# Performance work log

Measured on AMD Instinct MI355X. Metric: run time of the kernel, lower is better.

## Reference

```python
import jax, jax.numpy as jnp
import numpy as np

H = 512      # hidden_dim
OPS = 12     # num_ops
E = 112      # total_edges = num_cells * sum(i+2 for i in range(num_nodes)) = 8*14


def setup_inputs() -> dict:
    key = jax.random.key(0)
    ks = jax.random.split(key, 16)
    s = lambda k, shape: jax.random.normal(k, shape, dtype=jnp.float32) * 0.05
    return {
        "temperature": 1,
        "h0": s(ks[0], (2, H)),
        "c0": s(ks[1], (2, H)),
        "Wih0": s(ks[2], (4 * H, H)),
        "Whh0": s(ks[3], (4 * H, H)),
        "bih0": s(ks[4], (4 * H,)),
        "bhh0": s(ks[5], (4 * H,)),
        "Wih1": s(ks[6], (4 * H, H)),
        "Whh1": s(ks[7], (4 * H, H)),
        "bih1": s(ks[8], (4 * H,)),
        "bhh1": s(ks[9], (4 * H,)),
        "emb": s(ks[10], (OPS, H)),
        "cW1": s(ks[11], (E, H, H)),
        "cb1": s(ks[12], (E, H)),
        "cW2": s(ks[13], (E, H, OPS)),
        "cb2": s(ks[14], (E, OPS)),
    }


def _lstm_cell(x, h, c, Wih, Whh, bih, bhh):
    # PyTorch LSTM gate order: i, f, g, o
    gates = x @ Wih.T + bih + h @ Whh.T + bhh  # [4H]
    i, f, g, o = jnp.split(gates, 4)
    c2 = jax.nn.sigmoid(f) * c + jax.nn.sigmoid(i) * jnp.tanh(g)
    h2 = jax.nn.sigmoid(o) * jnp.tanh(c2)
    return h2, c2


def reference(temperature, h0, c0, Wih0, Whh0, bih0, bhh0,
              Wih1, Whh1, bih1, bhh1, emb, cW1, cb1, cW2, cb2):
    temp = jnp.asarray(temperature, jnp.float32)
    # Gumbel-max trick == torch Categorical sampling (fixed on-device noise)
    gumbel = jax.random.gumbel(jax.random.key(42), (E, OPS), dtype=jnp.float32)

    def step(carry, xs):
        h, c, prev_action = carry          # h, c: [2, H]
        idx, W1, b1, W2, b2, gnoise = xs
        x = jnp.where(idx == 0, jnp.zeros((H,), jnp.float32), emb[prev_action])
        h0n, c0n = _lstm_cell(x, h[0], c[0], Wih0, Whh0, bih0, bhh0)
        h1n, c1n = _lstm_cell(h0n, h[1], c[1], Wih1, Whh1, bih1, bhh1)
        hmlp = jax.nn.relu(h1n @ W1 + b1)   # controller hidden
        logits = (hmlp @ W2 + b2) / temp    # [OPS]
        logp = jax.nn.log_softmax(logits)
        action = jnp.argmax(logits + gnoise).astype(jnp.int32)
        lp = logp[action]
        ent = -jnp.sum(jnp.exp(logp) * logp)
        new_carry = (jnp.stack([h0n, h1n]), jnp.stack([c0n, c1n]), action)
        return new_carry, (action, lp, ent)

    init = (h0, c0, jnp.int32(0))
    xs = (jnp.arange(E), cW1, cb1, cW2, cb2, gumbel)
    _, (actions, log_probs, entropies) = jax.lax.scan(step, init, xs)
    return actions, log_probs, entropies
```

## Files before the change

kernel.cpp:

```cpp
#include <hip/hip_runtime.h>
#include <math.h>

#define H    512
#define OPS  12
#define E    112
#define NWG  128
#define NT   256

typedef unsigned long long u64;

#define TW_BASE  16
#define TW_HB0   0
#define TW_HB1   1024
#define TW_HMB   2048
#define TW_TOTAL 3072

__device__ __forceinline__ float sigf(float x) { return 1.f / (1.f + expf(-x)); }

__device__ __forceinline__ void threefry_42(unsigned x0, unsigned x1,
                                            unsigned& o0, unsigned& o1) {
  const unsigned k0 = 0u, k1 = 42u;
  const unsigned k2 = k0 ^ k1 ^ 0x1BD11BDAu;
  x0 += k0; x1 += k1;
#define TF_R(rot) { x0 += x1; x1 = (x1 << rot) | (x1 >> (32 - rot)); x1 ^= x0; }
  TF_R(13) TF_R(15) TF_R(26) TF_R(6)
  x0 += k1; x1 += k2 + 1u;
  TF_R(17) TF_R(29) TF_R(16) TF_R(24)
  x0 += k2; x1 += k0 + 2u;
  TF_R(13) TF_R(15) TF_R(26) TF_R(6)
  x0 += k0; x1 += k1 + 3u;
  TF_R(17) TF_R(29) TF_R(16) TF_R(24)
  x0 += k1; x1 += k2 + 4u;
  TF_R(13) TF_R(15) TF_R(26) TF_R(6)
  x0 += k2; x1 += k0 + 5u;
#undef TF_R
  o0 = x0; o1 = x1;
}

__device__ __forceinline__ float bits_to_gumbel(unsigned bits) {
  unsigned fb = (bits >> 9) | 0x3f800000u;
  float u = __uint_as_float(fb) - 1.0f;
  u = u + 1.17549435e-38f;
  u = fmaxf(1.17549435e-38f, u);
  return -logf(-logf(u));
}

__device__ __forceinline__ float decode_temp(const void* temp_p) {
  float tf = *(const float*)temp_p;
  float a = fabsf(tf);
  if (a > 1e-6f && a < 1e6f) return tf;
  int ti = *(const int*)temp_p;
  if (ti != 0 && ti > -1000000 && ti < 1000000) return (float)ti;
  double td = *(const double*)temp_p;
  double ad = fabs(td);
  if (ad > 1e-6 && ad < 1e6) return (float)td;
  return 1.0f;
}

__device__ __forceinline__ void tag_store(u64* p, unsigned tag, float f) {
  u64 v = ((u64)tag << 32) | (u64)__float_as_uint(f);
  __hip_atomic_store(p, v, __ATOMIC_RELAXED, __HIP_MEMORY_SCOPE_SYSTEM);
}
__device__ __forceinline__ float tag_poll(const u64* p, unsigned tag) {
  u64 v = __hip_atomic_load(p, __ATOMIC_RELAXED, __HIP_MEMORY_SCOPE_SYSTEM);
  while ((unsigned)(v >> 32) != tag) {
    __builtin_amdgcn_s_sleep(1);
    v = __hip_atomic_load(p, __ATOMIC_RELAXED, __HIP_MEMORY_SCOPE_SYSTEM);
  }
  return __uint_as_float((unsigned)v);
}

__global__ void k_init(u64* tw) {
  int t = blockIdx.x * blockDim.x + threadIdx.x;
  if (t < TW_TOTAL) tw[t] = 0ull;
}
__global__ void k_diag(float* out, float v) {
  if (threadIdx.x == 0 && blockIdx.x == 0) out[0] = v;
}

__global__ void __launch_bounds__(NT)
policy_persist(const void* temp_p,
               const float* __restrict__ h0_in, const float* __restrict__ c0_in,
               const float* __restrict__ Wih0,  const float* __restrict__ Whh0,
               const float* __restrict__ bih0,  const float* __restrict__ bhh0,
               const float* __restrict__ Wih1,  const float* __restrict__ Whh1,
               const float* __restrict__ bih1,  const float* __restrict__ bhh1,
               const float* __restrict__ emb,   const float* __restrict__ cW1,
               const float* __restrict__ cb1,   const float* __restrict__ cW2,
               const float* __restrict__ cb2,
               float* __restrict__ out, float* ws) {
  __shared__ __align__(16) float shp0[H], shp1[H], hm[H];
  __shared__ float g0pre[16], g1bpre[16], g1loc[16];
  __shared__ float ewloc[12 * 16], b0loc[16], b1loc[16];
  __shared__ float gum[E * OPS];
  __shared__ float w1s[512 * 5];
  __shared__ float w2s[512 * 13];
  __shared__ float c0loc[4], c1loc[4];
  __shared__ float spart[4][4];
  __shared__ int s_act;

  const int tid = threadIdx.x;
  const int bid = blockIdx.x;
  const int j0  = bid * 4;
  const int cb  = (bid & 7) * 16 + (bid >> 3);
  const float invt = 1.f / decode_temp(temp_p);

  u64* HB0 = (u64*)(ws + TW_BASE) + TW_HB0;
  u64* HB1 = (u64*)(ws + TW_BASE) + TW_HB1;
  u64* HMB = (u64*)(ws + TW_BASE) + TW_HMB;

  for (int p = tid; p < E * OPS; p += NT) {
    unsigned y0, y1;
    threefry_42(0u, (unsigned)p, y0, y1);
    gum[p] = bits_to_gumbel(y0 ^ y1);
  }
  for (int j = tid; j < H; j += NT) {
    shp0[j] = h0_in[j];
    shp1[j] = h0_in[H + j];
  }
  if (tid < 192) {
    int a = tid / 16, ridx = tid % 16;
    int g = ridx >> 2, dj = ridx & 3;
    int row = g * H + j0 + dj;
    const float* er = emb + a * H;
    const float* wr = Wih0 + (size_t)row * H;
    float acc = 0.f;
    for (int k = 0; k < H; k += 4) {
      float4 e4 = *(const float4*)(er + k);
      float4 w4 = *(const float4*)(wr + k);
      acc += e4.x * w4.x + e4.y * w4.y + e4.z * w4.z + e4.w * w4.w;
    }
    ewloc[tid] = acc;
  }
  if (tid < 16) {
    int g = tid >> 2, dj = tid & 3;
    int row = g * H + j0 + dj;
    b0loc[tid] = bih0[row] + bhh0[row];
    b1loc[tid] = bih1[row] + bhh1[row];
  }
  if (tid < 4) {
    c0loc[tid] = c0_in[j0 + tid];
    c1loc[tid] = c0_in[H + j0 + tid];
  }
  __syncthreads();

  {
    int rowidx = tid >> 3, lane = tid & 7;
    int cell = rowidx >> 4, ridx = rowidx & 15;
    int g = ridx >> 2, dj = ridx & 3;
    int row = g * H + j0 + dj;
    const float* wr = (cell ? Whh1 : Whh0) + (size_t)row * H + lane * 64;
    const float* hv = (cell ? shp1 : shp0) + lane * 64;
    float acc = 0.f;
#pragma unroll
    for (int k = 0; k < 64; k += 4) {
      float4 w4 = *(const float4*)(wr + k);
      acc += w4.x * hv[k] + w4.y * hv[k + 1] + w4.z * hv[k + 2] + w4.w * hv[k + 3];
    }
    acc += __shfl_xor(acc, 1);
    acc += __shfl_xor(acc, 2);
    acc += __shfl_xor(acc, 4);
    if (lane == 0) {
      if (cell == 0) g0pre[ridx] = acc + b0loc[ridx];
      else           g1bpre[ridx] = acc;
    }
    const float* wb = cW1 + (size_t)cb * 4;
    float4 r0 = *(const float4*)(wb + (size_t)tid * H);
    float4 r1 = *(const float4*)(wb + (size_t)(tid + 256) * H);
    int k0 = tid * 5, k1 = (tid + 256) * 5;
    w1s[k0] = r0.x; w1s[k0 + 1] = r0.y; w1s[k0 + 2] = r0.z; w1s[k0 + 3] = r0.w;
    w1s[k1] = r1.x; w1s[k1 + 1] = r1.y; w1s[k1 + 2] = r1.z; w1s[k1 + 3] = r1.w;
  }
  __syncthreads();

#pragma unroll 1
  for (int i = 0; i < E; ++i) {
    const int p = i & 1;
    const unsigned tg = (unsigned)(i + 1);

    if (i > 0) {
      const int q = (i - 1) & 1;
      const unsigned tgp = (unsigned)i;
      int t2 = tid * 2;
      hm[t2]     = tag_poll(&HMB[q * 512 + t2],     tgp);
      hm[t2 + 1] = tag_poll(&HMB[q * 512 + t2 + 1], tgp);
      __syncthreads();
      if (tid < 64) {
        float lg[OPS];
#pragma unroll
        for (int o = 0; o < OPS; ++o) lg[o] = 0.f;
#pragma unroll
        for (int jj = 0; jj < 8; ++jj) {
          int j = jj * 64 + tid;
          float hmv = hm[j];
          const float* w2r = &w2s[j * 13];
#pragma unroll
          for (int o = 0; o < OPS; ++o) lg[o] += hmv * w2r[o];
        }
#pragma unroll
        for (int s = 1; s < 64; s <<= 1) {
#pragma unroll
          for (int o = 0; o < OPS; ++o) lg[o] += __shfl_xor(lg[o], s);
        }
#pragma unroll
        for (int o = 0; o < OPS; ++o) lg[o] = (lg[o] + cb2[(i - 1) * OPS + o]) * invt;
        float mx = lg[0];
#pragma unroll
        for (int o = 1; o < OPS; ++o) mx = fmaxf(mx, lg[o]);
        float se = 0.f;
#pragma unroll
        for (int o = 0; o < OPS; ++o) se += expf(lg[o] - mx);
        float logZ = mx + logf(se);
        float best = -1e30f; int act = 0;
#pragma unroll
        for (int o = 0; o < OPS; ++o) {
          float v = lg[o] + gum[(i - 1) * OPS + o];
          if (v > best) { best = v; act = o; }
        }
        if (tid == 0) {
          s_act = act;
          if (bid == 0) {
            float lp = lg[act] - logZ;
            float ent = 0.f;
            for (int o = 0; o < OPS; ++o) {
              float l2 = lg[o] - logZ;
              ent -= expf(l2) * l2;
            }
            out[i - 1]         = (float)act;
            out[E + i - 1]     = lp;
            out[2 * E + i - 1] = ent;
          }
        }
      }
    }

    if (tid < 4) {
      int a = (i > 0) ? s_act : -1;
      float gi = g0pre[tid];
      float gf = g0pre[4 + tid];
      float gg = g0pre[8 + tid];
      float go = g0pre[12 + tid];
      if (a >= 0) {
        gi += ewloc[a * 16 + tid];
        gf += ewloc[a * 16 + 4 + tid];
        gg += ewloc[a * 16 + 8 + tid];
        go += ewloc[a * 16 + 12 + tid];
      }
      float cn = sigf(gf) * c0loc[tid] + sigf(gi) * tanhf(gg);
      c0loc[tid] = cn;
      tag_store(&HB0[p * 512 + j0 + tid], tg, sigf(go) * tanhf(cn));
    }

    {
      int t2 = tid * 2;
      shp0[t2]     = tag_poll(&HB0[p * 512 + t2],     tg);
      shp0[t2 + 1] = tag_poll(&HB0[p * 512 + t2 + 1], tg);
    }
    __syncthreads();

    {
      int ridx = tid >> 4, lane = tid & 15;
      int g = ridx >> 2, dj = ridx & 3;
      int row = g * H + j0 + dj;
      const float* wr = Wih1 + (size_t)row * H + lane * 32;
      const float* hv = shp0 + lane * 32;
      float acc = 0.f;
#pragma unroll
      for (int k = 0; k < 32; k += 4) {
        float4 w4 = *(const float4*)(wr + k);
        acc += w4.x * hv[k] + w4.y * hv[k + 1] + w4.z * hv[k + 2] + w4.w * hv[k + 3];
      }
      acc += __shfl_xor(acc, 1);
      acc += __shfl_xor(acc, 2);
      acc += __shfl_xor(acc, 4);
      acc += __shfl_xor(acc, 8);
      if (lane == 0) g1loc[ridx] = acc + g1bpre[ridx] + b1loc[ridx];
    }
    __syncthreads();

    if (tid < 4) {
      float gi = g1loc[tid];
      float gf = g1loc[4 + tid];
      float gg = g1loc[8 + tid];
      float go = g1loc[12 + tid];
      float cn = sigf(gf) * c1loc[tid] + sigf(gi) * tanhf(gg);
      c1loc[tid] = cn;
      tag_store(&HB1[p * 512 + j0 + tid], tg, sigf(go) * tanhf(cn));
    }

    {
      int t2 = tid * 2;
      shp1[t2]     = tag_poll(&HB1[p * 512 + t2],     tg);
      shp1[t2 + 1] = tag_poll(&HB1[p * 512 + t2 + 1], tg);
    }
    __syncthreads();

    {
      int wv = tid >> 6, ln = tid & 63;
      int jl = ln & 3, ks = ln >> 2;
      int kbase = wv * 128 + ks * 8;
      float acc = 0.f;
#pragma unroll
      for (int t = 0; t < 8; ++t) {
        int k = kbase + t;
        acc += shp1[k] * w1s[k * 5 + jl];
      }
      acc += __shfl_xor(acc, 4);
      acc += __shfl_xor(acc, 8);
      acc += __shfl_xor(acc, 16);
      acc += __shfl_xor(acc, 32);
      if (ln < 4) spart[wv][ln] = acc;
    }
    __syncthreads();
    if (tid < 4) {
      float s = spart[0][tid] + spart[1][tid] + spart[2][tid] + spart[3][tid];
      s += cb1[(size_t)i * H + cb * 4 + tid];
      tag_store(&HMB[p * 512 + cb * 4 + tid], tg, fmaxf(s, 0.f));
    }

    {
      const float* wsrc = cW2 + (size_t)i * H * OPS;
#pragma unroll
      for (int r = 0; r < 6; ++r) {
        int q = tid + 256 * r;
        float4 v = *(const float4*)(wsrc + 4 * q);
        int f = 4 * q;
        w2s[(f / 12) * 13 + (f % 12)]             = v.x;
        w2s[((f + 1) / 12) * 13 + ((f + 1) % 12)] = v.y;
        w2s[((f + 2) / 12) * 13 + ((f + 2) % 12)] = v.z;
        w2s[((f + 3) / 12) * 13 + ((f + 3) % 12)] = v.w;
      }
    }
    if (i + 1 < E) {
      const float* wb = cW1 + (size_t)(i + 1) * H * H + (size_t)cb * 4;
      float4 r0 = *(const float4*)(wb + (size_t)tid * H);
      float4 r1 = *(const float4*)(wb + (size_t)(tid + 256) * H);
      {
        int rowidx = tid >> 3, lane = tid & 7;
        int cell = rowidx >> 4, ridx = rowidx & 15;
        int g = ridx >> 2, dj = ridx & 3;
        int row = g * H + j0 + dj;
        const float* wr = (cell ? Whh1 : Whh0) + (size_t)row * H + lane * 64;
        const float* hv = (cell ? shp1 : shp0) + lane * 64;
        float acc = 0.f;
#pragma unroll
        for (int k = 0; k < 64; k += 4) {
          float4 w4 = *(const float4*)(wr + k);
          acc += w4.x * hv[k] + w4.y * hv[k + 1] + w4.z * hv[k + 2] + w4.w * hv[k + 3];
        }
        acc += __shfl_xor(acc, 1);
        acc += __shfl_xor(acc, 2);
        acc += __shfl_xor(acc, 4);
        if (lane == 0) {
          if (cell == 0) g0pre[ridx] = acc + b0loc[ridx];
          else           g1bpre[ridx] = acc;
        }
      }
      int k0 = tid * 5, k1 = (tid + 256) * 5;
      w1s[k0] = r0.x; w1s[k0 + 1] = r0.y; w1s[k0 + 2] = r0.z; w1s[k0 + 3] = r0.w;
      w1s[k1] = r1.x; w1s[k1 + 1] = r1.y; w1s[k1 + 2] = r1.z; w1s[k1 + 3] = r1.w;
    }
    __syncthreads();
  }

  if (bid == 0) {
    const int q = (E - 1) & 1;
    int t2 = tid * 2;
    hm[t2]     = tag_poll(&HMB[q * 512 + t2],     (unsigned)E);
    hm[t2 + 1] = tag_poll(&HMB[q * 512 + t2 + 1], (unsigned)E);
    __syncthreads();
    if (tid < 64) {
      float lg[OPS];
#pragma unroll
      for (int o = 0; o < OPS; ++o) lg[o] = 0.f;
#pragma unroll
      for (int jj = 0; jj < 8; ++jj) {
        int j = jj * 64 + tid;
        float hmv = hm[j];
        const float* w2r = &w2s[j * 13];
#pragma unroll
        for (int o = 0; o < OPS; ++o) lg[o] += hmv * w2r[o];
      }
#pragma unroll
      for (int s = 1; s < 64; s <<= 1) {
#pragma unroll
        for (int o = 0; o < OPS; ++o) lg[o] += __shfl_xor(lg[o], s);
      }
#pragma unroll
      for (int o = 0; o < OPS; ++o) lg[o] = (lg[o] + cb2[(E - 1) * OPS + o]) * invt;
      float mx = lg[0];
#pragma unroll
      for (int o = 1; o < OPS; ++o) mx = fmaxf(mx, lg[o]);
      float se = 0.f;
#pragma unroll
      for (int o = 0; o < OPS; ++o) se += expf(lg[o] - mx);
      float logZ = mx + logf(se);
      float best = -1e30f; int act = 0;
#pragma unroll
      for (int o = 0; o < OPS; ++o) {
        float v = lg[o] + gum[(E - 1) * OPS + o];
        if (v > best) { best = v; act = o; }
      }
      if (tid == 0) {
        float lp = lg[act] - logZ;
        float ent = 0.f;
        for (int o = 0; o < OPS; ++o) {
          float l2 = lg[o] - logZ;
          ent -= expf(l2) * l2;
        }
        out[E - 1]     = (float)act;
        out[2 * E - 1] = lp;
        out[3 * E - 1] = ent;
      }
    }
  }
}

extern "C" void kernel_launch(void* const* d_in, const int* in_sizes, int n_in,
                              void* d_out, int out_size, void* d_ws, size_t ws_size,
                              hipStream_t stream) {
  (void)out_size; (void)ws_size;
  float* out = (float*)d_out;
  float* ws  = (float*)d_ws;

  (void)hipGetLastError();

  static const long long expect[16] = {
      1, 1024, 1024, 1048576, 1048576, 2048, 2048,
      1048576, 1048576, 2048, 2048, 6144,
      29360128, 57344, 688128, 1344 };
  int bad = -1;
  if (n_in != 16) bad = 99;
  else {
    for (int i = 0; i < 16; ++i)
      if ((long long)in_sizes[i] != expect[i]) { bad = i; break; }
  }

  k_init<<<12, 256, 0, stream>>>((u64*)(ws + TW_BASE));
  if (bad >= 0) {
    k_diag<<<1, 64, 0, stream>>>(out, 80000.0f + (float)bad);
    return;
  }

  policy_persist<<<NWG, NT, 0, stream>>>(
      d_in[0],
      (const float*)d_in[1],  (const float*)d_in[2],
      (const float*)d_in[3],  (const float*)d_in[4],
      (const float*)d_in[5],  (const float*)d_in[6],
      (const float*)d_in[7],  (const float*)d_in[8],
      (const float*)d_in[9],  (const float*)d_in[10],
      (const float*)d_in[11], (const float*)d_in[12],
      (const float*)d_in[13], (const float*)d_in[14],
      (const float*)d_in[15],
      out, ws);

  hipError_t e = hipGetLastError();
  if (e != hipSuccess) {
    k_diag<<<1, 64, 0, stream>>>(out, 90000.0f + (float)(int)e);
  }
}
```

Baseline: 1.074 ms.

## Reorder LSTM step to overlap Whh0 recurrence and W1 prefetch, add W1 relayout

```diff
diff --git a/kernel.cpp b/kernel.cpp
--- a/kernel.cpp
+++ b/kernel.cpp
@@ -8,12 +8,13 @@
 #define NT   256
 
 typedef unsigned long long u64;
-
-#define TW_BASE  16
+typedef unsigned int u32x4 __attribute__((ext_vector_type(4)));
+
 #define TW_HB0   0
 #define TW_HB1   1024
 #define TW_HMB   2048
 #define TW_TOTAL 3072
+#define WS_W1T_F (16 + 2 * TW_TOTAL)
 
 __device__ __forceinline__ float sigf(float x) { return 1.f / (1.f + expf(-x)); }
 
@@ -61,13 +62,18 @@
   u64 v = ((u64)tag << 32) | (u64)__float_as_uint(f);
   __hip_atomic_store(p, v, __ATOMIC_RELAXED, __HIP_MEMORY_SCOPE_SYSTEM);
 }
-__device__ __forceinline__ float tag_poll(const u64* p, unsigned tag) {
-  u64 v = __hip_atomic_load(p, __ATOMIC_RELAXED, __HIP_MEMORY_SCOPE_SYSTEM);
-  while ((unsigned)(v >> 32) != tag) {
+__device__ __forceinline__ void tag_poll2(const u64* p, unsigned tag,
+                                          float& f0, float& f1) {
+  u32x4 v;
+  for (;;) {
+    asm volatile("global_load_dwordx4 %0, %1, off sc0 sc1\n\t"
+                 "s_waitcnt vmcnt(0)"
+                 : "=&v"(v) : "v"(p) : "memory");
+    if (v.y == tag && v.w == tag) break;
     __builtin_amdgcn_s_sleep(1);
-    v = __hip_atomic_load(p, __ATOMIC_RELAXED, __HIP_MEMORY_SCOPE_SYSTEM);
-  }
-  return __uint_as_float((unsigned)v);
+  }
+  f0 = __uint_as_float(v.x);
+  f1 = __uint_as_float(v.z);
 }
 
 __global__ void k_init(u64* tw) {
@@ -76,6 +82,19 @@
 }
 __global__ void k_diag(float* out, float v) {
   if (threadIdx.x == 0 && blockIdx.x == 0) out[0] = v;
+}
+
+__global__ void __launch_bounds__(NT)
+k_w1t(const float* __restrict__ cW1, float* __restrict__ w1t) {
+  int t = blockIdx.x * NT + threadIdx.x;
+  size_t e0 = (size_t)t * 4;
+  int i = (int)(e0 >> 18);
+  int rem = (int)(e0 & 262143);
+  int k = rem >> 9, j = rem & 511;
+  int b = j >> 4, jc = j & 15;
+  float4 v = *(const float4*)(cW1 + e0);
+  size_t dst = (((size_t)(i * 32 + b) * 512 + k) << 4) + jc;
+  *(float4*)(w1t + dst) = v;
 }
 
 __global__ void __launch_bounds__(NT)
@@ -88,8 +107,8 @@
                const float* __restrict__ emb,   const float* __restrict__ cW1,
                const float* __restrict__ cb1,   const float* __restrict__ cW2,
                const float* __restrict__ cb2,
-               float* __restrict__ out, float* ws) {
-  __shared__ __align__(16) float shp0[H], shp1[H], hm[H];
+               float* __restrict__ out, float* ws, int use_w1t) {
+  __shared__ __align__(16) float h0full[H], shp1[H], hm[H];
   __shared__ float g0pre[16], g1bpre[16], g1loc[16];
   __shared__ float ewloc[12 * 16], b0loc[16], b1loc[16];
   __shared__ float gum[E * OPS];
@@ -105,9 +124,11 @@
   const int cb  = (bid & 7) * 16 + (bid >> 3);
   const float invt = 1.f / decode_temp(temp_p);
 
-  u64* HB0 = (u64*)(ws + TW_BASE) + TW_HB0;
-  u64* HB1 = (u64*)(ws + TW_BASE) + TW_HB1;
-  u64* HMB = (u64*)(ws + TW_BASE) + TW_HMB;
+  u64* HB0 = (u64*)(ws + 16) + TW_HB0;
+  u64* HB1 = (u64*)(ws + 16) + TW_HB1;
+  u64* HMB = (u64*)(ws + 16) + TW_HMB;
+  const float* W1T = ws + WS_W1T_F;
+  const int bb = cb >> 2, boff = (cb & 3) * 4;
 
   for (int p = tid; p < E * OPS; p += NT) {
     unsigned y0, y1;
@@ -115,8 +136,8 @@
     gum[p] = bits_to_gumbel(y0 ^ y1);
   }
   for (int j = tid; j < H; j += NT) {
-    shp0[j] = h0_in[j];
-    shp1[j] = h0_in[H + j];
+    h0full[j] = h0_in[j];
+    shp1[j]   = h0_in[H + j];
   }
   if (tid < 192) {
     int a = tid / 16, ridx = tid % 16;
@@ -150,7 +171,7 @@
     int g = ridx >> 2, dj = ridx & 3;
     int row = g * H + j0 + dj;
     const float* wr = (cell ? Whh1 : Whh0) + (size_t)row * H + lane * 64;
-    const float* hv = (cell ? shp1 : shp0) + lane * 64;
+    const float* hv = (cell ? shp1 : h0full) + lane * 64;
     float acc = 0.f;
 #pragma unroll
     for (int k = 0; k < 64; k += 4) {
@@ -164,9 +185,16 @@
       if (cell == 0) g0pre[ridx] = acc + b0loc[ridx];
       else           g1bpre[ridx] = acc;
     }
-    const float* wb = cW1 + (size_t)cb * 4;
-    float4 r0 = *(const float4*)(wb + (size_t)tid * H);
-    float4 r1 = *(const float4*)(wb + (size_t)(tid + 256) * H);
+    float4 r0, r1;
+    if (use_w1t) {
+      const float* wt = W1T + (((size_t)bb * 512) << 4) + boff;
+      r0 = *(const float4*)(wt + ((size_t)tid << 4));
+      r1 = *(const float4*)(wt + ((size_t)(tid + 256) << 4));
+    } else {
+      const float* wb = cW1 + (size_t)cb * 4;
+      r0 = *(const float4*)(wb + (size_t)tid * H);
+      r1 = *(const float4*)(wb + (size_t)(tid + 256) * H);
+    }
     int k0 = tid * 5, k1 = (tid + 256) * 5;
     w1s[k0] = r0.x; w1s[k0 + 1] = r0.y; w1s[k0 + 2] = r0.z; w1s[k0 + 3] = r0.w;
     w1s[k1] = r1.x; w1s[k1 + 1] = r1.y; w1s[k1 + 2] = r1.z; w1s[k1 + 3] = r1.w;
@@ -180,10 +208,8 @@
 
     if (i > 0) {
       const int q = (i - 1) & 1;
-      const unsigned tgp = (unsigned)i;
       int t2 = tid * 2;
-      hm[t2]     = tag_poll(&HMB[q * 512 + t2],     tgp);
-      hm[t2 + 1] = tag_poll(&HMB[q * 512 + t2 + 1], tgp);
+      tag_poll2(&HMB[q * 512 + t2], (unsigned)i, hm[t2], hm[t2 + 1]);
       __syncthreads();
       if (tid < 64) {
         float lg[OPS];
@@ -253,8 +279,7 @@
 
     {
       int t2 = tid * 2;
-      shp0[t2]     = tag_poll(&HB0[p * 512 + t2],     tg);
-      shp0[t2 + 1] = tag_poll(&HB0[p * 512 + t2 + 1], tg);
+      tag_poll2(&HB0[p * 512 + t2], tg, h0full[t2], h0full[t2 + 1]);
     }
     __syncthreads();
 
@@ -263,7 +288,7 @@
       int g = ridx >> 2, dj = ridx & 3;
       int row = g * H + j0 + dj;
       const float* wr = Wih1 + (size_t)row * H + lane * 32;
-      const float* hv = shp0 + lane * 32;
+      const float* hv = h0full + lane * 32;
       float acc = 0.f;
 #pragma unroll
       for (int k = 0; k < 32; k += 4) {
@@ -288,36 +313,35 @@
       tag_store(&HB1[p * 512 + j0 + tid], tg, sigf(go) * tanhf(cn));
     }
 
-    {
-      int t2 = tid * 2;
-      shp1[t2]     = tag_poll(&HB1[p * 512 + t2],     tg);
-      shp1[t2 + 1] = tag_poll(&HB1[p * 512 + t2 + 1], tg);
-    }
-    __syncthreads();
-
-    {
-      int wv = tid >> 6, ln = tid & 63;
-      int jl = ln & 3, ks = ln >> 2;
-      int kbase = wv * 128 + ks * 8;
+    float4 v0, v1;
+    if (i + 1 < E) {
+      if (use_w1t) {
+        const float* wt = W1T + (((size_t)((i + 1) * 32 + bb) * 512) << 4) + boff;
+        v0 = *(const float4*)(wt + ((size_t)tid << 4));
+        v1 = *(const float4*)(wt + ((size_t)(tid + 256) << 4));
+      } else {
+        const float* wb = cW1 + (size_t)(i + 1) * H * H + (size_t)cb * 4;
+        v0 = *(const float4*)(wb + (size_t)tid * H);
+        v1 = *(const float4*)(wb + (size_t)(tid + 256) * H);
+      }
+    }
+    if (tid < 128) {
+      int ridx = tid >> 3, lane = tid & 7;
+      int g = ridx >> 2, dj = ridx & 3;
+      int row = g * H + j0 + dj;
+      const float* wr = Whh0 + (size_t)row * H + lane * 64;
+      const float* hv = h0full + lane * 64;
       float acc = 0.f;
 #pragma unroll
-      for (int t = 0; t < 8; ++t) {
-        int k = kbase + t;
-        acc += shp1[k] * w1s[k * 5 + jl];
-      }
+      for (int k = 0; k < 64; k += 4) {
+        float4 w4 = *(const float4*)(wr + k);
+        acc += w4.x * hv[k] + w4.y * hv[k + 1] + w4.z * hv[k + 2] + w4.w * hv[k + 3];
+      }
+      acc += __shfl_xor(acc, 1);
+      acc += __shfl_xor(acc, 2);
       acc += __shfl_xor(acc, 4);
-      acc += __shfl_xor(acc, 8);
-      acc += __shfl_xor(acc, 16);
-      acc += __shfl_xor(acc, 32);
-      if (ln < 4) spart[wv][ln] = acc;
-    }
-    __syncthreads();
-    if (tid < 4) {
-      float s = spart[0][tid] + spart[1][tid] + spart[2][tid] + spart[3][tid];
-      s += cb1[(size_t)i * H + cb * 4 + tid];
-      tag_store(&HMB[p * 512 + cb * 4 + tid], tg, fmaxf(s, 0.f));
-    }
-
+      if (lane == 0) g0pre[ridx] = acc + b0loc[ridx];
+    }
     {
       const float* wsrc = cW2 + (size_t)i * H * OPS;
 #pragma unroll
@@ -331,17 +355,43 @@
         w2s[((f + 3) / 12) * 13 + ((f + 3) % 12)] = v.w;
       }
     }
+
+    {
+      int t2 = tid * 2;
+      tag_poll2(&HB1[p * 512 + t2], tg, shp1[t2], shp1[t2 + 1]);
+    }
+    __syncthreads();
+
+    {
+      int wv = tid >> 6, ln = tid & 63;
+      int jl = ln & 3, ks = ln >> 2;
+      int kbase = wv * 128 + ks * 8;
+      float acc = 0.f;
+#pragma unroll
+      for (int t = 0; t < 8; ++t) {
+        int k = kbase + t;
+        acc += shp1[k] * w1s[k * 5 + jl];
+      }
+      acc += __shfl_xor(acc, 4);
+      acc += __shfl_xor(acc, 8);
+      acc += __shfl_xor(acc, 16);
+      acc += __shfl_xor(acc, 32);
+      if (ln < 4) spart[wv][ln] = acc;
+    }
+    __syncthreads();
+    if (tid < 4) {
+      float s = spart[0][tid] + spart[1][tid] + spart[2][tid] + spart[3][tid];
+      s += cb1[(size_t)i * H + cb * 4 + tid];
+      tag_store(&HMB[p * 512 + cb * 4 + tid], tg, fmaxf(s, 0.f));
+    }
+
     if (i + 1 < E) {
-      const float* wb = cW1 + (size_t)(i + 1) * H * H + (size_t)cb * 4;
-      float4 r0 = *(const float4*)(wb + (size_t)tid * H);
-      float4 r1 = *(const float4*)(wb + (size_t)(tid + 256) * H);
-      {
-        int rowidx = tid >> 3, lane = tid & 7;
-        int cell = rowidx >> 4, ridx = rowidx & 15;
+      if (tid < 128) {
+        int ridx = tid >> 3, lane = tid & 7;
         int g = ridx >> 2, dj = ridx & 3;
         int row = g * H + j0 + dj;
-        const float* wr = (cell ? Whh1 : Whh0) + (size_t)row * H + lane * 64;
-        const float* hv = (cell ? shp1 : shp0) + lane * 64;
+        const float* wr = Whh1 + (size_t)row * H + lane * 64;
+        const float* hv = shp1 + lane * 64;
         float acc = 0.f;
 #pragma unroll
         for (int k = 0; k < 64; k += 4) {
@@ -351,14 +401,11 @@
         acc += __shfl_xor(acc, 1);
         acc += __shfl_xor(acc, 2);
         acc += __shfl_xor(acc, 4);
-        if (lane == 0) {
-          if (cell == 0) g0pre[ridx] = acc + b0loc[ridx];
-          else           g1bpre[ridx] = acc;
-        }
+        if (lane == 0) g1bpre[ridx] = acc;
       }
       int k0 = tid * 5, k1 = (tid + 256) * 5;
-      w1s[k0] = r0.x; w1s[k0 + 1] = r0.y; w1s[k0 + 2] = r0.z; w1s[k0 + 3] = r0.w;
-      w1s[k1] = r1.x; w1s[k1 + 1] = r1.y; w1s[k1 + 2] = r1.z; w1s[k1 + 3] = r1.w;
+      w1s[k0] = v0.x; w1s[k0 + 1] = v0.y; w1s[k0 + 2] = v0.z; w1s[k0 + 3] = v0.w;
+      w1s[k1] = v1.x; w1s[k1 + 1] = v1.y; w1s[k1 + 2] = v1.z; w1s[k1 + 3] = v1.w;
     }
     __syncthreads();
   }
@@ -366,8 +413,7 @@
   if (bid == 0) {
     const int q = (E - 1) & 1;
     int t2 = tid * 2;
-    hm[t2]     = tag_poll(&HMB[q * 512 + t2],     (unsigned)E);
-    hm[t2 + 1] = tag_poll(&HMB[q * 512 + t2 + 1], (unsigned)E);
+    tag_poll2(&HMB[q * 512 + t2], (unsigned)E, hm[t2], hm[t2 + 1]);
     __syncthreads();
     if (tid < 64) {
       float lg[OPS];
@@ -419,7 +465,7 @@
 extern "C" void kernel_launch(void* const* d_in, const int* in_sizes, int n_in,
                               void* d_out, int out_size, void* d_ws, size_t ws_size,
                               hipStream_t stream) {
-  (void)out_size; (void)ws_size;
+  (void)out_size;
   float* out = (float*)d_out;
   float* ws  = (float*)d_ws;
 
@@ -436,10 +482,16 @@
       if ((long long)in_sizes[i] != expect[i]) { bad = i; break; }
   }
 
-  k_init<<<12, 256, 0, stream>>>((u64*)(ws + TW_BASE));
+  k_init<<<12, 256, 0, stream>>>((u64*)(ws + 16));
   if (bad >= 0) {
     k_diag<<<1, 64, 0, stream>>>(out, 80000.0f + (float)bad);
     return;
+  }
+
+  const size_t need = (size_t)WS_W1T_F * 4 + (size_t)29360128 * 4;
+  int use_w1t = (ws_size >= need) ? 1 : 0;
+  if (use_w1t) {
+    k_w1t<<<28672, 256, 0, stream>>>((const float*)d_in[12], ws + WS_W1T_F);
   }
 
   policy_persist<<<NWG, NT, 0, stream>>>(
@@ -452,7 +504,7 @@
       (const float*)d_in[11], (const float*)d_in[12],
       (const float*)d_in[13], (const float*)d_in[14],
       (const float*)d_in[15],
-      out, ws);
+      out, ws, use_w1t);
 
   hipError_t e = hipGetLastError();
   if (e != hipSuccess) {
```

Measured after the change: 1.142 ms. 1.06x slower.
